# Performance work log

Measured on AMD Instinct MI355X. Metric: run time of the kernel, lower is better.

Reference implementation:

```python
import jax, jax.numpy as jnp
import numpy as np

B, S, H = 2, 2048, 1024
G, HEADS = 4, 16
HPG = HEADS // G          # heads per group = 4
HD = H // HEADS           # head_dim = 64
DG = H // G               # per-group proj dim = 256
SCALE = 1.0 / np.sqrt(HD)


def setup_inputs() -> dict:
    key = jax.random.key(0)
    ks = jax.random.split(key, 6)
    w = 0.02
    return {
        "hidden_states": jax.random.normal(ks[0], (B, S, H), dtype=jnp.float32),
        "Wq": jax.random.normal(ks[1], (G, DG, H), dtype=jnp.float32) * w,
        "bq": jnp.zeros((G, DG), dtype=jnp.float32),
        "Wk": jax.random.normal(ks[2], (G, DG, H), dtype=jnp.float32) * w,
        "bk": jnp.zeros((G, DG), dtype=jnp.float32),
        "Wv": jax.random.normal(ks[3], (G, DG, H), dtype=jnp.float32) * w,
        "bv": jnp.zeros((G, DG), dtype=jnp.float32),
        "Wo": jax.random.normal(ks[4], (H, H), dtype=jnp.float32) * w,
        "bo": jnp.zeros((H,), dtype=jnp.float32),
    }


def _proj_split(x, W, b):
    # x: [B,S,H], W: [G,DG,H], b: [G,DG] -> [B,G,HPG,S,HD]
    y = jnp.einsum("bsh,gdh->bgsd", x, W) + b[None, :, None, :]
    y = y.reshape(x.shape[0], G, x.shape[1], HPG, HD)
    return jnp.transpose(y, (0, 1, 3, 2, 4))


def reference(hidden_states, Wq, bq, Wk, bk, Wv, bv, Wo, bo):
    q = _proj_split(hidden_states, Wq, bq)  # [B,G,HPG,S,HD]
    k = _proj_split(hidden_states, Wk, bk)
    v = _proj_split(hidden_states, Wv, bv)
    scores = jnp.einsum("bghqd,bghkd->bghqk", q, k) * SCALE
    attn = jax.nn.softmax(scores.astype(jnp.float32), axis=-1).astype(v.dtype)
    ctx = jnp.einsum("bghqk,bghkd->bghqd", attn, v)  # [B,G,HPG,S,HD]
    # merge: heads ordered group-major, matching torch cat over group dim
    ctx = jnp.transpose(ctx, (0, 3, 1, 2, 4)).reshape(hidden_states.shape[0], hidden_states.shape[1], H)
    return jnp.einsum("bsh,oh->bso", ctx, Wo) + bo
```

## Files before the change

### kernel.cpp

```cpp
#include <hip/hip_runtime.h>

typedef __bf16 bf16x8 __attribute__((ext_vector_type(8)));
typedef float f32x4 __attribute__((ext_vector_type(4)));
typedef float f32x16 __attribute__((ext_vector_type(16)));
typedef unsigned int uint4v __attribute__((ext_vector_type(4)));
typedef unsigned int uint2v __attribute__((ext_vector_type(2)));

#define LOG2E 1.4426950408889634f

static __device__ __forceinline__ unsigned short f2bf(float f) {
  union { float f; unsigned int u; } c; c.f = f;
  return (unsigned short)((c.u + 0x7fffu + ((c.u >> 16) & 1u)) >> 16);
}

static __device__ __forceinline__ void gload16(const void* g, void* l) {
  __builtin_amdgcn_global_load_lds(
      (const __attribute__((address_space(1))) void*)g,
      (__attribute__((address_space(3))) void*)l, 16, 0, 0);
}

static __device__ __forceinline__ float exp2fast(float x) {
#if __has_builtin(__builtin_amdgcn_exp2f)
  return __builtin_amdgcn_exp2f(x);
#else
  return exp2f(x);
#endif
}

static __device__ __forceinline__ f32x16 mfma32(bf16x8 a, bf16x8 b, f32x16 c) {
  return __builtin_amdgcn_mfma_f32_32x32x16_bf16(a, b, c, 0, 0, 0);
}

static __device__ __forceinline__ unsigned cvt_pk_bf16(float a, float b) {
  unsigned r;
  asm("v_cvt_pk_bf16_f32 %0, %1, %2" : "=v"(r) : "v"(a), "v"(b));
  return r;
}

static __device__ __forceinline__ void pl32_swap(unsigned& a, unsigned& b) {
#if __has_builtin(__builtin_amdgcn_permlane32_swap)
  uint2v r = __builtin_amdgcn_permlane32_swap(a, b, false, false);
  a = r[0]; b = r[1];
#else
  asm volatile("v_permlane32_swap_b32 %0, %1" : "+v"(a), "+v"(b));
#endif
}

__global__ void cvt_all(const float* __restrict__ x,
                        const float* __restrict__ Wq,
                        const float* __restrict__ Wk,
                        const float* __restrict__ Wv,
                        const float* __restrict__ Wo,
                        ushort4* __restrict__ dst) {
  int i = blockIdx.x * 256 + threadIdx.x;
  const float* src;
  int off;
  if (i < 1048576) {
    src = x; off = i;
  } else {
    int t = (i - 1048576) >> 18;
    off = (i - 1048576) & 262143;
    src = (t == 0) ? Wq : (t == 1) ? Wk : (t == 2) ? Wv : Wo;
  }
  float4 f = ((const float4*)src)[off];
  ushort4 o;
  o.x = f2bf(f.x); o.y = f2bf(f.y); o.z = f2bf(f.z); o.w = f2bf(f.w);
  dst[i] = o;
}

__launch_bounds__(256, 4)
__global__ void qkv_gemm(const unsigned short* __restrict__ xb,
                         const unsigned short* __restrict__ wq,
                         const unsigned short* __restrict__ wk,
                         const unsigned short* __restrict__ wv,
                         const float* __restrict__ bq,
                         const float* __restrict__ bk,
                         const float* __restrict__ bv,
                         unsigned short* __restrict__ Qo,
                         unsigned short* __restrict__ Ko,
                         unsigned short* __restrict__ VTo) {
  __shared__ unsigned short As[128 * 64];
  __shared__ unsigned short Bs[128 * 64];
  const int s0 = blockIdx.x * 128;
  const int n0g = blockIdx.y * 128;
  const int qkv = n0g >> 10;
  const int d0 = n0g & 1023;
  const unsigned short* W = (qkv == 0) ? wq : ((qkv == 1) ? wk : wv);
  const float* bias = (qkv == 0) ? bq : ((qkv == 1) ? bk : bv);

  const unsigned short* Aptr; const unsigned short* Bptr;
  int Aoff, Boff;
  if (qkv < 2) { Aptr = W;  Aoff = d0; Bptr = xb; Boff = s0; }
  else         { Aptr = xb; Aoff = s0; Bptr = W;  Boff = d0; }

  const int tid = threadIdx.x;
  const int lane = tid & 63;
  const int wid = tid >> 6;
  const int wm = (wid >> 1) * 64;
  const int wn = (wid & 1) * 64;
  const int lm = lane & 15;
  const int quad = lane >> 4;

  f32x4 acc[4][4] = {};

  for (int kk = 0; kk < 1024; kk += 64) {
#pragma unroll
    for (int t = 0; t < 4; ++t) {
      int i = t * 256 + tid;
      int row = i >> 3, tp = i & 7;
      int seg = tp ^ (row & 7);
      gload16(Aptr + (size_t)(Aoff + row) * 1024 + kk + seg * 8,
              As + (size_t)i * 8);
      gload16(Bptr + (size_t)(Boff + row) * 1024 + kk + seg * 8,
              Bs + (size_t)i * 8);
    }
    __syncthreads();
#pragma unroll
    for (int h = 0; h < 2; ++h) {
      bf16x8 af[4], bff[4];
#pragma unroll
      for (int mt = 0; mt < 4; ++mt) {
        int r = wm + mt * 16 + lm;
        af[mt] = *(const bf16x8*)(As + r * 64 + (((h * 4 + quad) ^ (r & 7)) * 8));
      }
#pragma unroll
      for (int nt = 0; nt < 4; ++nt) {
        int r = wn + nt * 16 + lm;
        bff[nt] = *(const bf16x8*)(Bs + r * 64 + (((h * 4 + quad) ^ (r & 7)) * 8));
      }
#pragma unroll
      for (int mt = 0; mt < 4; ++mt)
#pragma unroll
        for (int nt = 0; nt < 4; ++nt)
          acc[mt][nt] = __builtin_amdgcn_mfma_f32_16x16x32_bf16(
              af[mt], bff[nt], acc[mt][nt], 0, 0, 0);
    }
    __syncthreads();
  }

  if (qkv < 2) {
    unsigned short* OUT = (qkv == 0) ? Qo : Ko;
    const float scale = (qkv == 0) ? (0.125f * LOG2E) : 1.0f;
#pragma unroll
    for (int mt = 0; mt < 4; ++mt) {
      const int d = d0 + wm + mt * 16 + quad * 4;
      const int g = d >> 8, hpg = (d >> 6) & 3, hd = d & 63;
      const float4 bb = *(const float4*)(bias + d);
#pragma unroll
      for (int nt = 0; nt < 4; ++nt) {
        const int srow = s0 + wn + nt * 16 + lm;
        const int bidx = srow >> 11, s = srow & 2047;
        const int head = (bidx * 4 + g) * 4 + hpg;
        ushort4 o;
        o.x = f2bf((acc[mt][nt][0] + bb.x) * scale);
        o.y = f2bf((acc[mt][nt][1] + bb.y) * scale);
        o.z = f2bf((acc[mt][nt][2] + bb.z) * scale);
        o.w = f2bf((acc[mt][nt][3] + bb.w) * scale);
        *(ushort4*)(OUT + (size_t)head * 131072 + (size_t)s * 64 + hd) = o;
      }
    }
  } else {
#pragma unroll
    for (int nt = 0; nt < 4; ++nt) {
      const int d = d0 + wn + nt * 16 + lm;
      const int g = d >> 8, hpg = (d >> 6) & 3, hd = d & 63;
      const float bb = bias[d];
#pragma unroll
      for (int mt = 0; mt < 4; ++mt) {
        const int sbase = s0 + wm + mt * 16 + quad * 4;
        const int bidx = sbase >> 11, s = sbase & 2047;
        const int head = (bidx * 4 + g) * 4 + hpg;
        ushort4 o;
        o.x = f2bf(acc[mt][nt][0] + bb);
        o.y = f2bf(acc[mt][nt][1] + bb);
        o.z = f2bf(acc[mt][nt][2] + bb);
        o.w = f2bf(acc[mt][nt][3] + bb);
        *(ushort4*)(VTo + (size_t)head * 131072 + (size_t)hd * 2048 + s) = o;
      }
    }
  }
}

static __device__ __forceinline__ void stage_kv64(
    const unsigned short* Kh, const unsigned short* Vh, int kv0,
    unsigned short* ksl, unsigned short* vsl, int tid) {
#pragma unroll
  for (int t = 0; t < 2; ++t) {
    int i = t * 256 + tid;
    int r = i >> 3, j = i & 7;
    gload16(Kh + (size_t)(kv0 + r) * 64 + ((j ^ (r & 7)) << 3),
            ksl + (size_t)i * 8);
  }
#pragma unroll
  for (int t = 0; t < 2; ++t) {
    int i = t * 256 + tid;
    int r = i >> 3, j = i & 7;
    gload16(Vh + (size_t)r * 2048 + kv0 + ((j ^ (r & 7)) << 3),
            vsl + (size_t)i * 8);
  }
}

__launch_bounds__(256, 4)
__global__ void attn_kernel(const unsigned short* __restrict__ Q,
                            const unsigned short* __restrict__ K,
                            const unsigned short* __restrict__ VT,
                            unsigned short* __restrict__ ctx) {
  __shared__ __align__(16) unsigned char smem[32768];

  const int f = blockIdx.x;
  const int xcd = f & 7;
  const int idx = f >> 3;
  const int head = xcd * 4 + (idx & 3);
  const int q0 = (idx >> 2) * 64;
  const int b = head >> 4;
  const int colbase = (head & 15) * 64;

  const unsigned short* Qh = Q + (size_t)head * 131072;
  const unsigned short* Kh = K + (size_t)head * 131072;
  const unsigned short* Vh = VT + (size_t)head * 131072;

  const int tid = threadIdx.x;
  const int lane = tid & 63;
  const int w = tid >> 6;
  const int wq = w & 1;
  const int wkv = w >> 1;
  const int l31 = lane & 31;
  const int hi = lane >> 5;

  stage_kv64(Kh, Vh, 0, (unsigned short*)smem,
             (unsigned short*)(smem + 16384), tid);

  bf16x8 qf[4];
  {
    const size_t qrow = (size_t)(q0 + wq * 32 + l31);
#pragma unroll
    for (int s = 0; s < 4; ++s)
      qf[s] = *(const bf16x8*)(Qh + qrow * 64 + s * 16 + hi * 8);
  }

  int koff[4];
  {
    const int r = wkv * 32 + l31;
#pragma unroll
    for (int s = 0; s < 4; ++s) {
      const int c = s * 2 + hi;
      koff[s] = r * 64 + ((c ^ (r & 7)) << 3);
    }
  }
  int voff[2][2];
#pragma unroll
  for (int db = 0; db < 2; ++db) {
    const int r = db * 32 + l31;
#pragma unroll
    for (int t = 0; t < 2; ++t) {
      const int c = wkv * 4 + t * 2 + hi;
      voff[db][t] = r * 64 + ((c ^ (r & 7)) << 3);
    }
  }

  __syncthreads();

  float psum = 0.f;
  f32x16 oacc[2] = {};

  for (int it = 0; it < 32; ++it) {
    const int buf = it & 1;
    const unsigned short* kbuf = (const unsigned short*)(smem + buf * 8192);
    const unsigned short* vbuf =
        (const unsigned short*)(smem + 16384 + buf * 8192);
    if (it < 31)
      stage_kv64(Kh, Vh, (it + 1) * 64,
                 (unsigned short*)(smem + (buf ^ 1) * 8192),
                 (unsigned short*)(smem + 16384 + (buf ^ 1) * 8192), tid);

    bf16x8 kf[4], vf[2][2];
#pragma unroll
    for (int s = 0; s < 4; ++s)
      kf[s] = *(const bf16x8*)(kbuf + koff[s]);
#pragma unroll
    for (int db = 0; db < 2; ++db)
#pragma unroll
      for (int t = 0; t < 2; ++t)
        vf[db][t] = *(const bf16x8*)(vbuf + voff[db][t]);

    f32x16 sc = {};
#pragma unroll
    for (int s = 0; s < 4; ++s)
      sc = mfma32(kf[s], qf[s], sc);

    float e[16];
#pragma unroll
    for (int r = 0; r < 16; ++r) e[r] = exp2fast(sc[r]);
    {
      float t0 = (e[0] + e[1]) + (e[2] + e[3]);
      float t1 = (e[4] + e[5]) + (e[6] + e[7]);
      float t2 = (e[8] + e[9]) + (e[10] + e[11]);
      float t3 = (e[12] + e[13]) + (e[14] + e[15]);
      psum += (t0 + t1) + (t2 + t3);
    }
    unsigned p[8];
#pragma unroll
    for (int j = 0; j < 8; ++j) p[j] = cvt_pk_bf16(e[2 * j], e[2 * j + 1]);
    pl32_swap(p[0], p[2]); pl32_swap(p[1], p[3]);
    pl32_swap(p[4], p[6]); pl32_swap(p[5], p[7]);
    uint4v u0 = {p[0], p[1], p[2], p[3]};
    uint4v u1 = {p[4], p[5], p[6], p[7]};
    const bf16x8 B0 = __builtin_bit_cast(bf16x8, u0);
    const bf16x8 B1 = __builtin_bit_cast(bf16x8, u1);
#pragma unroll
    for (int db = 0; db < 2; ++db) {
      oacc[db] = mfma32(vf[db][0], B0, oacc[db]);
      oacc[db] = mfma32(vf[db][1], B1, oacc[db]);
    }
    __syncthreads();
  }

  psum += __shfl_xor(psum, 32, 64);

  float* red = (float*)smem;
  float* psred = (float*)(smem + 17408);
  const int qi = wq * 32 + l31;
  if (wkv == 1) {
    if (hi == 0) psred[qi] = psum;
#pragma unroll
    for (int db = 0; db < 2; ++db)
#pragma unroll
      for (int g = 0; g < 4; ++g) {
        f32x4 ov;
        ov[0] = oacc[db][4 * g + 0];
        ov[1] = oacc[db][4 * g + 1];
        ov[2] = oacc[db][4 * g + 2];
        ov[3] = oacc[db][4 * g + 3];
        *(f32x4*)(red + qi * 68 + db * 32 + g * 8 + hi * 4) = ov;
      }
  }
  __syncthreads();
  if (wkv == 0) {
    const float inv = 1.0f / (psum + psred[qi]);
    const size_t row = (size_t)(b * 2048 + q0 + qi);
#pragma unroll
    for (int db = 0; db < 2; ++db)
#pragma unroll
      for (int g = 0; g < 4; ++g) {
        f32x4 o = *(const f32x4*)(red + qi * 68 + db * 32 + g * 8 + hi * 4);
        ushort4 st;
        st.x = f2bf((o[0] + oacc[db][4 * g + 0]) * inv);
        st.y = f2bf((o[1] + oacc[db][4 * g + 1]) * inv);
        st.z = f2bf((o[2] + oacc[db][4 * g + 2]) * inv);
        st.w = f2bf((o[3] + oacc[db][4 * g + 3]) * inv);
        *(ushort4*)(ctx + row * 1024 + colbase + db * 32 + g * 8 + hi * 4) = st;
      }
  }
}

__launch_bounds__(256, 4)
__global__ void out_gemm(const unsigned short* __restrict__ A,
                         const unsigned short* __restrict__ Wb,
                         const float* __restrict__ bo,
                         float* __restrict__ out) {
  __shared__ unsigned short As[128 * 64];
  __shared__ unsigned short Bs[64 * 64];
  const int s0 = blockIdx.x * 64;
  const int o0 = blockIdx.y * 128;

  const int tid = threadIdx.x;
  const int lane = tid & 63;
  const int wid = tid >> 6;
  const int wm = (wid >> 1) * 64;
  const int wn = (wid & 1) * 32;
  const int lm = lane & 15;
  const int quad = lane >> 4;

  f32x4 acc[4][2] = {};

  for (int kk = 0; kk < 1024; kk += 64) {
#pragma unroll
    for (int t = 0; t < 4; ++t) {
      int i = t * 256 + tid;
      int row = i >> 3, tp = i & 7;
      int seg = tp ^ (row & 7);
      gload16(Wb + (size_t)(o0 + row) * 1024 + kk + seg * 8, As + (size_t)i * 8);
    }
#pragma unroll
    for (int t = 0; t < 2; ++t) {
      int i = t * 256 + tid;
      int row = i >> 3, tp = i & 7;
      int seg = tp ^ (row & 7);
      gload16(A + (size_t)(s0 + row) * 1024 + kk + seg * 8, Bs + (size_t)i * 8);
    }
    __syncthreads();
#pragma unroll
    for (int h = 0; h < 2; ++h) {
      bf16x8 af[4], bff[2];
#pragma unroll
      for (int mt = 0; mt < 4; ++mt) {
        int r = wm + mt * 16 + lm;
        af[mt] = *(const bf16x8*)(As + r * 64 + (((h * 4 + quad) ^ (r & 7)) * 8));
      }
#pragma unroll
      for (int nt = 0; nt < 2; ++nt) {
        int r = wn + nt * 16 + lm;
        bff[nt] = *(const bf16x8*)(Bs + r * 64 + (((h * 4 + quad) ^ (r & 7)) * 8));
      }
#pragma unroll
      for (int mt = 0; mt < 4; ++mt)
#pragma unroll
        for (int nt = 0; nt < 2; ++nt)
          acc[mt][nt] = __builtin_amdgcn_mfma_f32_16x16x32_bf16(
              af[mt], bff[nt], acc[mt][nt], 0, 0, 0);
    }
    __syncthreads();
  }

#pragma unroll
  for (int mt = 0; mt < 4; ++mt) {
    const int o = o0 + wm + mt * 16 + quad * 4;
    const float4 bb = *(const float4*)(bo + o);
#pragma unroll
    for (int nt = 0; nt < 2; ++nt) {
      const int s = s0 + wn + nt * 16 + lm;
      float4 v;
      v.x = acc[mt][nt][0] + bb.x;
      v.y = acc[mt][nt][1] + bb.y;
      v.z = acc[mt][nt][2] + bb.z;
      v.w = acc[mt][nt][3] + bb.w;
      *(float4*)(out + (size_t)s * 1024 + o) = v;
    }
  }
}

extern "C" void kernel_launch(void* const* d_in, const int* in_sizes, int n_in,
                              void* d_out, int out_size, void* d_ws, size_t ws_size,
                              hipStream_t stream) {
  const float* x  = (const float*)d_in[0];
  const float* Wq = (const float*)d_in[1];
  const float* bq = (const float*)d_in[2];
  const float* Wk = (const float*)d_in[3];
  const float* bk = (const float*)d_in[4];
  const float* Wv = (const float*)d_in[5];
  const float* bv = (const float*)d_in[6];
  const float* Wo = (const float*)d_in[7];
  const float* bo = (const float*)d_in[8];
  float* out = (float*)d_out;

  char* ws = (char*)d_ws;
  unsigned short* xb  = (unsigned short*)(ws + 0);
  unsigned short* wqb = (unsigned short*)(ws + 8388608);
  unsigned short* wkb = (unsigned short*)(ws + 10485760);
  unsigned short* wvb = (unsigned short*)(ws + 12582912);
  unsigned short* wob = (unsigned short*)(ws + 14680064);
  unsigned short* Qb  = (unsigned short*)(ws + 16777216);
  unsigned short* Kb  = (unsigned short*)(ws + 25165824);
  unsigned short* VTb = (unsigned short*)(ws + 33554432);
  unsigned short* ctxb= (unsigned short*)(ws + 41943040);
  if (ws_size < 50331648) return;

  cvt_all<<<8192, 256, 0, stream>>>(x, Wq, Wk, Wv, Wo, (ushort4*)ws);
  qkv_gemm<<<dim3(32, 24), 256, 0, stream>>>(xb, wqb, wkb, wvb, bq, bk, bv,
                                             Qb, Kb, VTb);
  attn_kernel<<<dim3(1024), 256, 0, stream>>>(Qb, Kb, VTb, ctxb);
  out_gemm<<<dim3(64, 8), 256, 0, stream>>>(ctxb, wob, bo, out);
}
```

Before: 182.1 us.

## Enlarge attention tile to 128 queries and 128-key stages with 512 threads

The attention kernel now has 512-thread blocks, each covering 128 query rows instead of 64, and stages 128 keys per double-buffered iteration instead of 64. Each of the 8 waves processes two 32-key sub-blocks per iteration, so there are half as many barriers and each staged K/V tile is reused by more query waves. V is laid out in LDS with a 16-wide XOR swizzle to match the 128-wide rows. Shared memory doubles to 64KB per block and the grid halves to 512 blocks, which may lower occupancy and leave fewer blocks to balance across CUs.

```diff
diff --git a/kernel.cpp b/kernel.cpp
--- a/kernel.cpp
+++ b/kernel.cpp
@@ -181,37 +181,37 @@
   }
 }
 
-static __device__ __forceinline__ void stage_kv64(
+static __device__ __forceinline__ void stage_kv(
     const unsigned short* Kh, const unsigned short* Vh, int kv0,
     unsigned short* ksl, unsigned short* vsl, int tid) {
 #pragma unroll
   for (int t = 0; t < 2; ++t) {
-    int i = t * 256 + tid;
+    int i = t * 512 + tid;
     int r = i >> 3, j = i & 7;
     gload16(Kh + (size_t)(kv0 + r) * 64 + ((j ^ (r & 7)) << 3),
             ksl + (size_t)i * 8);
   }
 #pragma unroll
   for (int t = 0; t < 2; ++t) {
-    int i = t * 256 + tid;
-    int r = i >> 3, j = i & 7;
-    gload16(Vh + (size_t)r * 2048 + kv0 + ((j ^ (r & 7)) << 3),
+    int i = t * 512 + tid;
+    int r = i >> 4, j = i & 15;
+    gload16(Vh + (size_t)r * 2048 + kv0 + ((j ^ (r & 15)) << 3),
             vsl + (size_t)i * 8);
   }
 }
 
-__launch_bounds__(256, 4)
+__launch_bounds__(512, 4)
 __global__ void attn_kernel(const unsigned short* __restrict__ Q,
                             const unsigned short* __restrict__ K,
                             const unsigned short* __restrict__ VT,
                             unsigned short* __restrict__ ctx) {
-  __shared__ __align__(16) unsigned char smem[32768];
+  __shared__ __align__(16) unsigned char smem[65536];
 
   const int f = blockIdx.x;
   const int xcd = f & 7;
   const int idx = f >> 3;
   const int head = xcd * 4 + (idx & 3);
-  const int q0 = (idx >> 2) * 64;
+  const int q0 = (idx >> 2) * 128;
   const int b = head >> 4;
   const int colbase = (head & 15) * 64;
 
@@ -222,13 +222,13 @@
   const int tid = threadIdx.x;
   const int lane = tid & 63;
   const int w = tid >> 6;
-  const int wq = w & 1;
-  const int wkv = w >> 1;
+  const int wq = w & 3;
+  const int wkv = w >> 2;
   const int l31 = lane & 31;
   const int hi = lane >> 5;
 
-  stage_kv64(Kh, Vh, 0, (unsigned short*)smem,
-             (unsigned short*)(smem + 16384), tid);
+  stage_kv(Kh, Vh, 0, (unsigned short*)smem,
+           (unsigned short*)(smem + 32768), tid);
 
   bf16x8 qf[4];
   {
@@ -238,79 +238,85 @@
       qf[s] = *(const bf16x8*)(Qh + qrow * 64 + s * 16 + hi * 8);
   }
 
-  int koff[4];
-  {
-    const int r = wkv * 32 + l31;
+  int koff[2][4];
+#pragma unroll
+  for (int kb = 0; kb < 2; ++kb) {
+    const int r = wkv * 64 + kb * 32 + l31;
 #pragma unroll
     for (int s = 0; s < 4; ++s) {
       const int c = s * 2 + hi;
-      koff[s] = r * 64 + ((c ^ (r & 7)) << 3);
-    }
-  }
-  int voff[2][2];
-#pragma unroll
-  for (int db = 0; db < 2; ++db) {
-    const int r = db * 32 + l31;
-#pragma unroll
-    for (int t = 0; t < 2; ++t) {
-      const int c = wkv * 4 + t * 2 + hi;
-      voff[db][t] = r * 64 + ((c ^ (r & 7)) << 3);
-    }
-  }
+      koff[kb][s] = r * 64 + ((c ^ (r & 7)) << 3);
+    }
+  }
+  int voff[2][2][2];
+#pragma unroll
+  for (int kb = 0; kb < 2; ++kb)
+#pragma unroll
+    for (int db = 0; db < 2; ++db) {
+      const int r = db * 32 + l31;
+#pragma unroll
+      for (int t = 0; t < 2; ++t) {
+        const int c = wkv * 8 + kb * 4 + t * 2 + hi;
+        voff[kb][db][t] = r * 128 + ((c ^ (r & 15)) << 3);
+      }
+    }
 
   __syncthreads();
 
   float psum = 0.f;
   f32x16 oacc[2] = {};
 
-  for (int it = 0; it < 32; ++it) {
+  for (int it = 0; it < 16; ++it) {
     const int buf = it & 1;
-    const unsigned short* kbuf = (const unsigned short*)(smem + buf * 8192);
+    const unsigned short* kbuf = (const unsigned short*)(smem + buf * 16384);
     const unsigned short* vbuf =
-        (const unsigned short*)(smem + 16384 + buf * 8192);
-    if (it < 31)
-      stage_kv64(Kh, Vh, (it + 1) * 64,
-                 (unsigned short*)(smem + (buf ^ 1) * 8192),
-                 (unsigned short*)(smem + 16384 + (buf ^ 1) * 8192), tid);
-
-    bf16x8 kf[4], vf[2][2];
-#pragma unroll
-    for (int s = 0; s < 4; ++s)
-      kf[s] = *(const bf16x8*)(kbuf + koff[s]);
-#pragma unroll
-    for (int db = 0; db < 2; ++db)
-#pragma unroll
-      for (int t = 0; t < 2; ++t)
-        vf[db][t] = *(const bf16x8*)(vbuf + voff[db][t]);
-
-    f32x16 sc = {};
-#pragma unroll
-    for (int s = 0; s < 4; ++s)
-      sc = mfma32(kf[s], qf[s], sc);
-
-    float e[16];
-#pragma unroll
-    for (int r = 0; r < 16; ++r) e[r] = exp2fast(sc[r]);
-    {
-      float t0 = (e[0] + e[1]) + (e[2] + e[3]);
-      float t1 = (e[4] + e[5]) + (e[6] + e[7]);
-      float t2 = (e[8] + e[9]) + (e[10] + e[11]);
-      float t3 = (e[12] + e[13]) + (e[14] + e[15]);
-      psum += (t0 + t1) + (t2 + t3);
-    }
-    unsigned p[8];
-#pragma unroll
-    for (int j = 0; j < 8; ++j) p[j] = cvt_pk_bf16(e[2 * j], e[2 * j + 1]);
-    pl32_swap(p[0], p[2]); pl32_swap(p[1], p[3]);
-    pl32_swap(p[4], p[6]); pl32_swap(p[5], p[7]);
-    uint4v u0 = {p[0], p[1], p[2], p[3]};
-    uint4v u1 = {p[4], p[5], p[6], p[7]};
-    const bf16x8 B0 = __builtin_bit_cast(bf16x8, u0);
-    const bf16x8 B1 = __builtin_bit_cast(bf16x8, u1);
-#pragma unroll
-    for (int db = 0; db < 2; ++db) {
-      oacc[db] = mfma32(vf[db][0], B0, oacc[db]);
-      oacc[db] = mfma32(vf[db][1], B1, oacc[db]);
+        (const unsigned short*)(smem + 32768 + buf * 16384);
+    if (it < 15)
+      stage_kv(Kh, Vh, (it + 1) * 128,
+               (unsigned short*)(smem + (buf ^ 1) * 16384),
+               (unsigned short*)(smem + 32768 + (buf ^ 1) * 16384), tid);
+
+#pragma unroll
+    for (int kb = 0; kb < 2; ++kb) {
+      bf16x8 kf[4], vf[2][2];
+#pragma unroll
+      for (int s = 0; s < 4; ++s)
+        kf[s] = *(const bf16x8*)(kbuf + koff[kb][s]);
+#pragma unroll
+      for (int db = 0; db < 2; ++db)
+#pragma unroll
+        for (int t = 0; t < 2; ++t)
+          vf[db][t] = *(const bf16x8*)(vbuf + voff[kb][db][t]);
+
+      f32x16 sc = {};
+#pragma unroll
+      for (int s = 0; s < 4; ++s)
+        sc = mfma32(kf[s], qf[s], sc);
+
+      float e[16];
+#pragma unroll
+      for (int r = 0; r < 16; ++r) e[r] = exp2fast(sc[r]);
+      {
+        float t0 = (e[0] + e[1]) + (e[2] + e[3]);
+        float t1 = (e[4] + e[5]) + (e[6] + e[7]);
+        float t2 = (e[8] + e[9]) + (e[10] + e[11]);
+        float t3 = (e[12] + e[13]) + (e[14] + e[15]);
+        psum += (t0 + t1) + (t2 + t3);
+      }
+      unsigned p[8];
+#pragma unroll
+      for (int j = 0; j < 8; ++j) p[j] = cvt_pk_bf16(e[2 * j], e[2 * j + 1]);
+      pl32_swap(p[0], p[2]); pl32_swap(p[1], p[3]);
+      pl32_swap(p[4], p[6]); pl32_swap(p[5], p[7]);
+      uint4v u0 = {p[0], p[1], p[2], p[3]};
+      uint4v u1 = {p[4], p[5], p[6], p[7]};
+      const bf16x8 B0 = __builtin_bit_cast(bf16x8, u0);
+      const bf16x8 B1 = __builtin_bit_cast(bf16x8, u1);
+#pragma unroll
+      for (int db = 0; db < 2; ++db) {
+        oacc[db] = mfma32(vf[db][0], B0, oacc[db]);
+        oacc[db] = mfma32(vf[db][1], B1, oacc[db]);
+      }
     }
     __syncthreads();
   }
@@ -318,7 +324,7 @@
   psum += __shfl_xor(psum, 32, 64);
 
   float* red = (float*)smem;
-  float* psred = (float*)(smem + 17408);
+  float* psred = (float*)(smem + 34816);
   const int qi = wq * 32 + l31;
   if (wkv == 1) {
     if (hi == 0) psred[qi] = psum;
@@ -458,6 +464,6 @@
   cvt_all<<<8192, 256, 0, stream>>>(x, Wq, Wk, Wv, Wo, (ushort4*)ws);
   qkv_gemm<<<dim3(32, 24), 256, 0, stream>>>(xb, wqb, wkb, wvb, bq, bk, bv,
                                              Qb, Kb, VTb);
-  attn_kernel<<<dim3(1024), 256, 0, stream>>>(Qb, Kb, VTb, ctxb);
+  attn_kernel<<<dim3(512), 512, 0, stream>>>(Qb, Kb, VTb, ctxb);
   out_gemm<<<dim3(64, 8), 256, 0, stream>>>(ctxb, wob, bo, out);
 }
```

New measurement: 178.2 us. -2.1%, faster.
